# Kernel tuning notes

Measured on AMD Instinct MI355X. Metric: run time of the kernel, lower is better.

Reference implementation:

```python
import jax, jax.numpy as jnp
import numpy as np

NUM_TAGS = 32            # init arg
N = NUM_TAGS + 2         # internal num_tags (start/end appended)
START = N - 2
END = N - 1
B = 1024
T = 1024
NEG = -6969.0            # module's 'minus infinity' constant


def setup_inputs() -> dict:
    key = jax.random.key(0)
    k1, k2 = jax.random.split(key)
    features = jax.random.normal(k1, (B, T, N), dtype=jnp.float32)
    # learned parameter: transition matrix [N, N]
    transitions = jax.random.normal(k2, (N, N), dtype=jnp.float32)
    return {"features": features, "transitions": transitions}


def _viterbi(features, transitions):
    # features: [B, T, N]; transitions: [N, N]
    Bn, Tn, Nn = features.shape
    init = jnp.full((Bn, Nn), NEG, dtype=features.dtype).at[:, START].set(0.0)

    def step(scores, feat):
        # score[b, j, k] = scores[b, k] + feat[b, j] + transitions[j, k]
        sc = scores[:, None, :] + feat[:, :, None] + transitions[None, :, :]
        return jnp.max(sc, axis=-1), jnp.argmax(sc, axis=-1)

    feats_t = jnp.swapaxes(features, 0, 1)            # [T, B, N]
    scores, paths = jax.lax.scan(step, init, feats_t)  # paths: [T, B, N] int

    scores = scores + transitions[END]                # add transition to end tag
    best = jnp.max(scores, axis=-1)                   # [B]
    idx = jnp.argmax(scores, axis=-1)                 # [B]

    # backtrack through backpointers, from t = T-1 down to 0
    def back(i, path):
        ni = jnp.take_along_axis(path, i[:, None], axis=1)[:, 0]
        return ni, ni

    _, tags = jax.lax.scan(back, idx, paths, reverse=True)  # tags: [T, B]
    best_path = jnp.concatenate([tags.T, idx[:, None]], axis=1)  # [B, T+1]
    return best, best_path


def reference(features, transitions):
    return _viterbi(features, transitions)
```

## Files before the change

kernel.cpp:

```cpp
#include <hip/hip_runtime.h>
#include <stdint.h>

#define BB 1024
#define TT 1024
#define NN 34
#define NP 36
#define NB 2
#define TPB (NB * 136)
#define NEGV -6969.0f
#define PADV -1.0e30f

template<int C>
__device__ __forceinline__ int dpp_i(int x) {
    return __builtin_amdgcn_update_dpp(0, x, C, 0xF, 0xF, true);
}
template<int C>
__device__ __forceinline__ float dpp_f(float x) {
    return __int_as_float(dpp_i<C>(__float_as_int(x)));
}

__device__ __forceinline__ void lds_barrier() {
    asm volatile("s_waitcnt lgkmcnt(0)\n\ts_barrier" ::: "memory");
}

__global__ __launch_bounds__(TPB, 3) void viterbi_full(
        const float* __restrict__ feat,
        const float* __restrict__ trans,
        unsigned char* __restrict__ bpg,
        float* __restrict__ out)
{
    __shared__ float sbuf[2][NB][NP];
    __shared__ float fsb[NB][NN];
    __shared__ unsigned char Fm[NB][16][NN];
    __shared__ int Eb[NB][16];
    __shared__ int idxs[NB];

    const int tid = threadIdx.x;
    const int bl  = (tid >= 136) ? 1 : 0;
    const int r   = tid - bl * 136;
    const int j   = r >> 2;
    const int h   = r & 3;
    const int k0  = h * 9;
    const int bg  = blockIdx.x * NB + bl;

    for (int e = tid; e < 2 * NB * NP; e += TPB) {
        int kk = e % NP;
        ((float*)sbuf)[e] = (kk >= NN) ? PADV : ((kk == 32) ? 0.0f : NEGV);
    }

    float tr[9];
    int   kreg[9];
#pragma unroll
    for (int i = 0; i < 9; ++i) {
        int k = k0 + i;
        tr[i]   = (k < NN) ? trans[j * NN + k] : 0.0f;
        kreg[i] = k;
    }
    const float trE = (r < NN) ? trans[33 * NN + r] : 0.0f;

    const float* fp = feat + (size_t)bg * TT * NN + j;
    unsigned char* bpt = bpg + (size_t)bg * TT * NN + j;

    float fr0 = fp[0 * NN], fr1 = fp[1 * NN], fr2 = fp[2 * NN], fr3 = fp[3 * NN];

    float* const s0 = &sbuf[0][bl][0];
    float* const s1 = &sbuf[1][bl][0];

    __syncthreads();

    auto vstep = [&](const float* __restrict__ srd, float* __restrict__ swr,
                     float fv, unsigned char* bpw) {
        float vv[9];
#pragma unroll
        for (int i = 0; i < 9; ++i) vv[i] = (srd[k0 + i] + fv) + tr[i];
        float m = fmaxf(fmaxf(fmaxf(vv[0], vv[1]), fmaxf(vv[2], vv[3])),
                        fmaxf(fmaxf(vv[4], vv[5]), fmaxf(vv[6], vv[7])));
        m = fmaxf(m, vv[8]);
        m = fmaxf(m, dpp_f<0xB1>(m));
        m = fmaxf(m, dpp_f<0x4E>(m));
        int am = 127;
#pragma unroll
        for (int i = 8; i >= 0; --i) am = (vv[i] == m) ? kreg[i] : am;
        int ao = dpp_i<0xB1>(am); am = (ao < am) ? ao : am;
        ao = dpp_i<0x4E>(am);     am = (ao < am) ? ao : am;
        if (h == 0) { swr[j] = m; *bpw = (unsigned char)am; }
        lds_barrier();
    };

    for (int n = 0; n < 255; ++n) {
        { float f = fr0; fr0 = fp[4 * NN]; vstep(s0, s1, f, bpt + 0 * NN); }
        { float f = fr1; fr1 = fp[5 * NN]; vstep(s1, s0, f, bpt + 1 * NN); }
        { float f = fr2; fr2 = fp[6 * NN]; vstep(s0, s1, f, bpt + 2 * NN); }
        { float f = fr3; fr3 = fp[7 * NN]; vstep(s1, s0, f, bpt + 3 * NN); }
        fp += 4 * NN; bpt += 4 * NN;
    }
    vstep(s0, s1, fr0, bpt + 0 * NN);
    vstep(s1, s0, fr1, bpt + 1 * NN);
    vstep(s0, s1, fr2, bpt + 2 * NN);
    vstep(s1, s0, fr3, bpt + 3 * NN);

    if (r < NN) fsb[bl][r] = s0[r] + trE;
    __syncthreads();
    if (r == 0) {
        float bm = fsb[bl][0]; int bi = 0;
        for (int k = 1; k < NN; ++k) {
            float v = fsb[bl][k];
            if (v > bm) { bm = v; bi = k; }
        }
        out[bg] = bm; idxs[bl] = bi;
    }
    __syncthreads();

    const unsigned char* __restrict__ bb = bpg + (size_t)bg * TT * NN;

    {
        int g = (r >= 102) ? 3 : ((r >= 68) ? 2 : ((r >= 34) ? 1 : 0));
        int x = r - 34 * g;
        int c0 = g, c1 = g + 4, c2 = g + 8, c3 = g + 12;
        int m0 = x, m1 = x, m2 = x, m3 = x;
        for (int i = 63; i >= 0; --i) {
            m0 = bb[(size_t)((c0 * 64 + i) * NN) + m0];
            m1 = bb[(size_t)((c1 * 64 + i) * NN) + m1];
            m2 = bb[(size_t)((c2 * 64 + i) * NN) + m2];
            m3 = bb[(size_t)((c3 * 64 + i) * NN) + m3];
        }
        Fm[bl][c0][x] = m0; Fm[bl][c1][x] = m1;
        Fm[bl][c2][x] = m2; Fm[bl][c3][x] = m3;
    }
    __syncthreads();

    if (r == 0) {
        int e = idxs[bl];
        Eb[bl][15] = e;
        for (int c = 15; c >= 1; --c) { e = Fm[bl][c][e]; Eb[bl][c - 1] = e; }
    }
    __syncthreads();

    float* po = out + BB + (size_t)bg * (TT + 1);
    if (r < 16) {
        int c = r;
        int m = Eb[bl][c];
        for (int i = 63; i >= 0; --i) {
            m = bb[(size_t)((c * 64 + i) * NN) + m];
            po[c * 64 + i] = (float)m;
        }
    }
    if (r == 16) po[TT] = (float)idxs[bl];
}

extern "C" void kernel_launch(void* const* d_in, const int* in_sizes, int n_in,
                              void* d_out, int out_size, void* d_ws, size_t ws_size,
                              hipStream_t stream) {
    const float* feat  = (const float*)d_in[0];
    const float* trans = (const float*)d_in[1];
    float* out = (float*)d_out;
    unsigned char* bp = (unsigned char*)d_ws;

    viterbi_full<<<BB / NB, TPB, 0, stream>>>(feat, trans, bp, out);
}
```

Baseline: 547.3 us.

## Defer argmax off the critical path and vectorize LDS score loads

The per-step backpointer argmax is moved into the next step, where it is computed while that step's score loads from LDS are in flight. Only the max and the score write stay on the serial dependency chain between barriers. Each of the four lanes per tag now reads an overlapping 10-wide window at stride 8, fetched with float4/float2 LDS loads, which replaces the 9 scalar loads per lane. This adds registers for the carried previous values, plus a flush after the loop, in exchange for a shorter latency chain per timestep.

```diff
diff --git a/kernel.cpp b/kernel.cpp
--- a/kernel.cpp
+++ b/kernel.cpp
@@ -23,13 +23,15 @@
     asm volatile("s_waitcnt lgkmcnt(0)\n\ts_barrier" ::: "memory");
 }
 
+__device__ __forceinline__ int imin2(int a, int b) { return a < b ? a : b; }
+
 __global__ __launch_bounds__(TPB, 3) void viterbi_full(
         const float* __restrict__ feat,
         const float* __restrict__ trans,
         unsigned char* __restrict__ bpg,
         float* __restrict__ out)
 {
-    __shared__ float sbuf[2][NB][NP];
+    __shared__ __align__(16) float sbuf[2][NB][NP];
     __shared__ float fsb[NB][NN];
     __shared__ unsigned char Fm[NB][16][NN];
     __shared__ int Eb[NB][16];
@@ -40,7 +42,7 @@
     const int r   = tid - bl * 136;
     const int j   = r >> 2;
     const int h   = r & 3;
-    const int k0  = h * 9;
+    const int kw  = h << 3;
     const int bg  = blockIdx.x * NB + bl;
 
     for (int e = tid; e < 2 * NB * NP; e += TPB) {
@@ -48,14 +50,9 @@
         ((float*)sbuf)[e] = (kk >= NN) ? PADV : ((kk == 32) ? 0.0f : NEGV);
     }
 
-    float tr[9];
-    int   kreg[9];
+    float tr[10];
 #pragma unroll
-    for (int i = 0; i < 9; ++i) {
-        int k = k0 + i;
-        tr[i]   = (k < NN) ? trans[j * NN + k] : 0.0f;
-        kreg[i] = k;
-    }
+    for (int i = 0; i < 10; ++i) tr[i] = trans[j * NN + kw + i];
     const float trE = (r < NN) ? trans[33 * NN + r] : 0.0f;
 
     const float* fp = feat + (size_t)bg * TT * NN + j;
@@ -66,24 +63,51 @@
     float* const s0 = &sbuf[0][bl][0];
     float* const s1 = &sbuf[1][bl][0];
 
+    float pvv[10];
+#pragma unroll
+    for (int i = 0; i < 10; ++i) pvv[i] = 0.0f;
+    float pm = -1.0e30f;
+    unsigned char* pbp = bpt;
+
     __syncthreads();
+
+    auto amax_flush = [&]() {
+        int e[10];
+#pragma unroll
+        for (int i = 0; i < 10; ++i) e[i] = (pvv[i] == pm) ? (kw + i) : 127;
+        int a0 = imin2(e[0], e[1]), a1 = imin2(e[2], e[3]);
+        int a2 = imin2(e[4], e[5]), a3 = imin2(e[6], e[7]);
+        int a4 = imin2(e[8], e[9]);
+        int am = imin2(imin2(imin2(a0, a1), imin2(a2, a3)), a4);
+        int ao = dpp_i<0xB1>(am); am = imin2(ao, am);
+        ao = dpp_i<0x4E>(am);     am = imin2(ao, am);
+        if (h == 0) *pbp = (unsigned char)am;
+    };
 
     auto vstep = [&](const float* __restrict__ srd, float* __restrict__ swr,
                      float fv, unsigned char* bpw) {
-        float vv[9];
+        const float4 va = *reinterpret_cast<const float4*>(srd + kw);
+        const float4 vb = *reinterpret_cast<const float4*>(srd + kw + 4);
+        const float2 vc = *reinterpret_cast<const float2*>(srd + kw + 8);
+        amax_flush();
+        float sv[10];
+        sv[0] = va.x; sv[1] = va.y; sv[2] = va.z; sv[3] = va.w;
+        sv[4] = vb.x; sv[5] = vb.y; sv[6] = vb.z; sv[7] = vb.w;
+        sv[8] = vc.x; sv[9] = vc.y;
+        float vv[10];
 #pragma unroll
-        for (int i = 0; i < 9; ++i) vv[i] = (srd[k0 + i] + fv) + tr[i];
-        float m = fmaxf(fmaxf(fmaxf(vv[0], vv[1]), fmaxf(vv[2], vv[3])),
-                        fmaxf(fmaxf(vv[4], vv[5]), fmaxf(vv[6], vv[7])));
-        m = fmaxf(m, vv[8]);
+        for (int i = 0; i < 10; ++i) vv[i] = (sv[i] + fv) + tr[i];
+        float t0 = fmaxf(vv[0], vv[1]), t1 = fmaxf(vv[2], vv[3]);
+        float t2 = fmaxf(vv[4], vv[5]), t3 = fmaxf(vv[6], vv[7]);
+        float t4 = fmaxf(vv[8], vv[9]);
+        float m = fmaxf(fmaxf(fmaxf(t0, t1), fmaxf(t2, t3)), t4);
         m = fmaxf(m, dpp_f<0xB1>(m));
         m = fmaxf(m, dpp_f<0x4E>(m));
-        int am = 127;
+        if (h == 0) swr[j] = m;
 #pragma unroll
-        for (int i = 8; i >= 0; --i) am = (vv[i] == m) ? kreg[i] : am;
-        int ao = dpp_i<0xB1>(am); am = (ao < am) ? ao : am;
-        ao = dpp_i<0x4E>(am);     am = (ao < am) ? ao : am;
-        if (h == 0) { swr[j] = m; *bpw = (unsigned char)am; }
+        for (int i = 0; i < 10; ++i) pvv[i] = vv[i];
+        pm = m;
+        pbp = bpw;
         lds_barrier();
     };
 
@@ -98,6 +122,7 @@
     vstep(s1, s0, fr1, bpt + 1 * NN);
     vstep(s0, s1, fr2, bpt + 2 * NN);
     vstep(s1, s0, fr3, bpt + 3 * NN);
+    amax_flush();
 
     if (r < NN) fsb[bl][r] = s0[r] + trE;
     __syncthreads();
```

After: 561.5 us. +2.6%, slower.

## Map each batch element to one wavefront and drop block barriers from Viterbi scan

Applied to the files above, without the earlier changes.

Restructures the forward Viterbi recursion so a single 64-lane wavefront handles one sequence, with each lane owning one target tag and reducing over all 34 source tags in registers. The old scheme split each tag's reduction across 4 lanes with DPP shuffles and a block-wide barrier per time step. The new scheme exchanges scores through per-wave LDS with no s_barrier, relying on wave-synchronous execution. It also widens the backtrack-composition phase so each lane tracks 9 start tags. This trades roughly four times more ALU work per lane, and idle lanes 34-63, for removing the per-step barrier and cross-lane reductions.

```diff
diff --git a/kernel.cpp b/kernel.cpp
--- a/kernel.cpp
+++ b/kernel.cpp
@@ -4,148 +4,176 @@
 #define BB 1024
 #define TT 1024
 #define NN 34
-#define NP 36
-#define NB 2
-#define TPB (NB * 136)
 #define NEGV -6969.0f
-#define PADV -1.0e30f
 
-template<int C>
-__device__ __forceinline__ int dpp_i(int x) {
-    return __builtin_amdgcn_update_dpp(0, x, C, 0xF, 0xF, true);
-}
-template<int C>
-__device__ __forceinline__ float dpp_f(float x) {
-    return __int_as_float(dpp_i<C>(__float_as_int(x)));
+typedef float v2f __attribute__((ext_vector_type(2)));
+typedef float v4f __attribute__((ext_vector_type(4)));
+
+__device__ __forceinline__ float fmax3(float a, float b, float c) {
+    return fmaxf(fmaxf(a, b), c);
 }
 
-__device__ __forceinline__ void lds_barrier() {
-    asm volatile("s_waitcnt lgkmcnt(0)\n\ts_barrier" ::: "memory");
-}
-
-__global__ __launch_bounds__(TPB, 3) void viterbi_full(
+__global__ __launch_bounds__(256, 1) void viterbi_wave(
         const float* __restrict__ feat,
         const float* __restrict__ trans,
         unsigned char* __restrict__ bpg,
         float* __restrict__ out)
 {
-    __shared__ float sbuf[2][NB][NP];
-    __shared__ float fsb[NB][NN];
-    __shared__ unsigned char Fm[NB][16][NN];
-    __shared__ int Eb[NB][16];
-    __shared__ int idxs[NB];
+    __shared__ __align__(16) float sc[4][64];
+    __shared__ unsigned char Fm[4][16][NN];
+    __shared__ int Eb[4][16];
 
-    const int tid = threadIdx.x;
-    const int bl  = (tid >= 136) ? 1 : 0;
-    const int r   = tid - bl * 136;
-    const int j   = r >> 2;
-    const int h   = r & 3;
-    const int k0  = h * 9;
-    const int bg  = blockIdx.x * NB + bl;
+    const int wid  = threadIdx.x >> 6;
+    const int lane = threadIdx.x & 63;
+    const int j    = lane;
+    const int jm   = (j < NN) ? j : (NN - 1);
+    const bool act = (j < NN);
+    const int bg   = blockIdx.x * 4 + wid;
 
-    for (int e = tid; e < 2 * NB * NP; e += TPB) {
-        int kk = e % NP;
-        ((float*)sbuf)[e] = (kk >= NN) ? PADV : ((kk == 32) ? 0.0f : NEGV);
+    v4f t4[8]; v2f t2;
+    {
+        const float* trow = trans + jm * NN;
+#pragma unroll
+        for (int i = 0; i < 8; ++i)
+            t4[i] = (v4f){trow[4*i], trow[4*i+1], trow[4*i+2], trow[4*i+3]};
+        t2 = (v2f){trow[32], trow[33]};
+    }
+    v4f e4[8]; v2f e2;
+    {
+        const float* erow = trans + (NN - 1) * NN;
+#pragma unroll
+        for (int i = 0; i < 8; ++i)
+            e4[i] = (v4f){erow[4*i], erow[4*i+1], erow[4*i+2], erow[4*i+3]};
+        e2 = (v2f){erow[32], erow[33]};
     }
 
-    float tr[9];
-    int   kreg[9];
-#pragma unroll
-    for (int i = 0; i < 9; ++i) {
-        int k = k0 + i;
-        tr[i]   = (k < NN) ? trans[j * NN + k] : 0.0f;
-        kreg[i] = k;
-    }
-    const float trE = (r < NN) ? trans[33 * NN + r] : 0.0f;
-
-    const float* fp = feat + (size_t)bg * TT * NN + j;
+    const float* fp = feat + (size_t)bg * TT * NN + jm;
     unsigned char* bpt = bpg + (size_t)bg * TT * NN + j;
 
-    float fr0 = fp[0 * NN], fr1 = fp[1 * NN], fr2 = fp[2 * NN], fr3 = fp[3 * NN];
+    float* const scW = &sc[wid][0];
+    const v4f* const S4 = (const v4f*)scW;
+    const v2f* const S2 = (const v2f*)scW;
 
-    float* const s0 = &sbuf[0][bl][0];
-    float* const s1 = &sbuf[1][bl][0];
+    scW[lane] = (lane == 32) ? 0.0f : NEGV;
 
-    __syncthreads();
+    v4f q[8]; v2f q8;
+#pragma unroll
+    for (int i = 0; i < 8; ++i) q[i] = S4[i];
+    q8 = S2[16];
 
-    auto vstep = [&](const float* __restrict__ srd, float* __restrict__ swr,
-                     float fv, unsigned char* bpw) {
-        float vv[9];
+    float fr0 = fp[0*NN], fr1 = fp[1*NN], fr2 = fp[2*NN], fr3 = fp[3*NN];
+
+    auto vstep = [&](float fv, unsigned char* bpw) {
+        const v4f f4 = (v4f){fv, fv, fv, fv};
+        const v2f f2 = (v2f){fv, fv};
+        v4f w[8]; v2f w8;
 #pragma unroll
-        for (int i = 0; i < 9; ++i) vv[i] = (srd[k0 + i] + fv) + tr[i];
-        float m = fmaxf(fmaxf(fmaxf(vv[0], vv[1]), fmaxf(vv[2], vv[3])),
-                        fmaxf(fmaxf(vv[4], vv[5]), fmaxf(vv[6], vv[7])));
-        m = fmaxf(m, vv[8]);
-        m = fmaxf(m, dpp_f<0xB1>(m));
-        m = fmaxf(m, dpp_f<0x4E>(m));
+        for (int i = 0; i < 8; ++i) w[i] = (q[i] + f4) + t4[i];
+        w8 = (q8 + f2) + t2;
+        float wv[NN];
+#pragma unroll
+        for (int i = 0; i < 8; ++i) {
+            wv[4*i+0] = w[i].x; wv[4*i+1] = w[i].y;
+            wv[4*i+2] = w[i].z; wv[4*i+3] = w[i].w;
+        }
+        wv[32] = w8.x; wv[33] = w8.y;
+        float a[12];
+#pragma unroll
+        for (int i = 0; i < 11; ++i) a[i] = fmax3(wv[3*i], wv[3*i+1], wv[3*i+2]);
+        a[11] = wv[33];
+        float b0 = fmax3(a[0], a[1], a[2]), b1 = fmax3(a[3], a[4], a[5]);
+        float b2 = fmax3(a[6], a[7], a[8]), b3 = fmax3(a[9], a[10], a[11]);
+        float m = fmaxf(fmaxf(b0, b1), fmaxf(b2, b3));
+        scW[lane] = m;
+#pragma unroll
+        for (int i = 0; i < 8; ++i) q[i] = S4[i];
+        q8 = S2[16];
         int am = 127;
 #pragma unroll
-        for (int i = 8; i >= 0; --i) am = (vv[i] == m) ? kreg[i] : am;
-        int ao = dpp_i<0xB1>(am); am = (ao < am) ? ao : am;
-        ao = dpp_i<0x4E>(am);     am = (ao < am) ? ao : am;
-        if (h == 0) { swr[j] = m; *bpw = (unsigned char)am; }
-        lds_barrier();
+        for (int k = NN - 1; k >= 0; --k) am = (wv[k] == m) ? k : am;
+        if (act) *bpw = (unsigned char)am;
     };
 
     for (int n = 0; n < 255; ++n) {
-        { float f = fr0; fr0 = fp[4 * NN]; vstep(s0, s1, f, bpt + 0 * NN); }
-        { float f = fr1; fr1 = fp[5 * NN]; vstep(s1, s0, f, bpt + 1 * NN); }
-        { float f = fr2; fr2 = fp[6 * NN]; vstep(s0, s1, f, bpt + 2 * NN); }
-        { float f = fr3; fr3 = fp[7 * NN]; vstep(s1, s0, f, bpt + 3 * NN); }
-        fp += 4 * NN; bpt += 4 * NN;
+        { float f = fr0; fr0 = fp[4*NN]; vstep(f, bpt + 0*NN); }
+        { float f = fr1; fr1 = fp[5*NN]; vstep(f, bpt + 1*NN); }
+        { float f = fr2; fr2 = fp[6*NN]; vstep(f, bpt + 2*NN); }
+        { float f = fr3; fr3 = fp[7*NN]; vstep(f, bpt + 3*NN); }
+        fp += 4*NN; bpt += 4*NN;
     }
-    vstep(s0, s1, fr0, bpt + 0 * NN);
-    vstep(s1, s0, fr1, bpt + 1 * NN);
-    vstep(s0, s1, fr2, bpt + 2 * NN);
-    vstep(s1, s0, fr3, bpt + 3 * NN);
+    vstep(fr0, bpt + 0*NN);
+    vstep(fr1, bpt + 1*NN);
+    vstep(fr2, bpt + 2*NN);
+    vstep(fr3, bpt + 3*NN);
 
-    if (r < NN) fsb[bl][r] = s0[r] + trE;
-    __syncthreads();
-    if (r == 0) {
-        float bm = fsb[bl][0]; int bi = 0;
-        for (int k = 1; k < NN; ++k) {
-            float v = fsb[bl][k];
-            if (v > bm) { bm = v; bi = k; }
+    int bi;
+    float bm;
+    {
+        v4f w[8]; v2f w8;
+#pragma unroll
+        for (int i = 0; i < 8; ++i) w[i] = q[i] + e4[i];
+        w8 = q8 + e2;
+        float wv[NN];
+#pragma unroll
+        for (int i = 0; i < 8; ++i) {
+            wv[4*i+0] = w[i].x; wv[4*i+1] = w[i].y;
+            wv[4*i+2] = w[i].z; wv[4*i+3] = w[i].w;
         }
-        out[bg] = bm; idxs[bl] = bi;
+        wv[32] = w8.x; wv[33] = w8.y;
+        float a[12];
+#pragma unroll
+        for (int i = 0; i < 11; ++i) a[i] = fmax3(wv[3*i], wv[3*i+1], wv[3*i+2]);
+        a[11] = wv[33];
+        float b0 = fmax3(a[0], a[1], a[2]), b1 = fmax3(a[3], a[4], a[5]);
+        float b2 = fmax3(a[6], a[7], a[8]), b3 = fmax3(a[9], a[10], a[11]);
+        bm = fmaxf(fmaxf(b0, b1), fmaxf(b2, b3));
+        bi = 127;
+#pragma unroll
+        for (int k = NN - 1; k >= 0; --k) bi = (wv[k] == bm) ? k : bi;
     }
-    __syncthreads();
+    if (lane == 0) out[bg] = bm;
 
+    asm volatile("s_waitcnt vmcnt(0)" ::: "memory");
     const unsigned char* __restrict__ bb = bpg + (size_t)bg * TT * NN;
 
     {
-        int g = (r >= 102) ? 3 : ((r >= 68) ? 2 : ((r >= 34) ? 1 : 0));
-        int x = r - 34 * g;
-        int c0 = g, c1 = g + 4, c2 = g + 8, c3 = g + 12;
-        int m0 = x, m1 = x, m2 = x, m3 = x;
+        const int c = lane >> 2;
+        const int sub = lane & 3;
+        int mv[9];
+#pragma unroll
+        for (int qi = 0; qi < 9; ++qi) {
+            int x = sub + 4 * qi;
+            mv[qi] = (x < NN) ? x : (NN - 1);
+        }
+        const unsigned char* cb = bb + (size_t)c * 64 * NN;
         for (int i = 63; i >= 0; --i) {
-            m0 = bb[(size_t)((c0 * 64 + i) * NN) + m0];
-            m1 = bb[(size_t)((c1 * 64 + i) * NN) + m1];
-            m2 = bb[(size_t)((c2 * 64 + i) * NN) + m2];
-            m3 = bb[(size_t)((c3 * 64 + i) * NN) + m3];
+            const unsigned char* rb = cb + (size_t)i * NN;
+#pragma unroll
+            for (int qi = 0; qi < 9; ++qi) mv[qi] = rb[mv[qi]];
         }
-        Fm[bl][c0][x] = m0; Fm[bl][c1][x] = m1;
-        Fm[bl][c2][x] = m2; Fm[bl][c3][x] = m3;
+#pragma unroll
+        for (int qi = 0; qi < 9; ++qi) {
+            int x = sub + 4 * qi;
+            if (x < NN) Fm[wid][c][x] = (unsigned char)mv[qi];
+        }
     }
-    __syncthreads();
 
-    if (r == 0) {
-        int e = idxs[bl];
-        Eb[bl][15] = e;
-        for (int c = 15; c >= 1; --c) { e = Fm[bl][c][e]; Eb[bl][c - 1] = e; }
+    if (lane == 0) {
+        int e = bi;
+        Eb[wid][15] = e;
+        for (int c = 15; c >= 1; --c) { e = Fm[wid][c][e]; Eb[wid][c - 1] = e; }
     }
-    __syncthreads();
 
     float* po = out + BB + (size_t)bg * (TT + 1);
-    if (r < 16) {
-        int c = r;
-        int m = Eb[bl][c];
+    if (lane < 16) {
+        int c = lane;
+        int m = Eb[wid][c];
         for (int i = 63; i >= 0; --i) {
             m = bb[(size_t)((c * 64 + i) * NN) + m];
             po[c * 64 + i] = (float)m;
         }
     }
-    if (r == 16) po[TT] = (float)idxs[bl];
+    if (lane == 16) po[TT] = (float)bi;
 }
 
 extern "C" void kernel_launch(void* const* d_in, const int* in_sizes, int n_in,
@@ -156,5 +184,5 @@
     float* out = (float*)d_out;
     unsigned char* bp = (unsigned char*)d_ws;
 
-    viterbi_full<<<BB / NB, TPB, 0, stream>>>(feat, trans, bp, out);
+    viterbi_wave<<<BB / 4, 256, 0, stream>>>(feat, trans, bp, out);
 }
```

After: 626.8 us. 1.15x slower.

## Process two batch rows per thread instead of per thread group

Applied to the files above, without the earlier changes.

Before, each block ran 272 threads, one 136-thread group per batch row. Now each block has 136 threads and every thread handles both rows, interleaving their independent max/argmax chains inside each step. This is meant to halve the threads per batch and give each thread two independent dependency chains to hide LDS and DPP latency. The cost is roughly double the register use per thread (launch bounds lowered from 3 to 2) and longer per-step work on the serial critical path.

```diff
diff --git a/kernel.cpp b/kernel.cpp
--- a/kernel.cpp
+++ b/kernel.cpp
@@ -6,7 +6,7 @@
 #define NN 34
 #define NP 36
 #define NB 2
-#define TPB (NB * 136)
+#define TPB 136
 #define NEGV -6969.0f
 #define PADV -1.0e30f
 
@@ -23,7 +23,7 @@
     asm volatile("s_waitcnt lgkmcnt(0)\n\ts_barrier" ::: "memory");
 }
 
-__global__ __launch_bounds__(TPB, 3) void viterbi_full(
+__global__ __launch_bounds__(TPB, 2) void viterbi_full(
         const float* __restrict__ feat,
         const float* __restrict__ trans,
         unsigned char* __restrict__ bpg,
@@ -35,15 +35,13 @@
     __shared__ int Eb[NB][16];
     __shared__ int idxs[NB];
 
-    const int tid = threadIdx.x;
-    const int bl  = (tid >= 136) ? 1 : 0;
-    const int r   = tid - bl * 136;
+    const int r   = threadIdx.x;
     const int j   = r >> 2;
     const int h   = r & 3;
     const int k0  = h * 9;
-    const int bg  = blockIdx.x * NB + bl;
+    const int bg0 = blockIdx.x * NB;
 
-    for (int e = tid; e < 2 * NB * NP; e += TPB) {
+    for (int e = r; e < 2 * NB * NP; e += TPB) {
         int kk = e % NP;
         ((float*)sbuf)[e] = (kk >= NN) ? PADV : ((kk == 32) ? 0.0f : NEGV);
     }
@@ -58,94 +56,131 @@
     }
     const float trE = (r < NN) ? trans[33 * NN + r] : 0.0f;
 
-    const float* fp = feat + (size_t)bg * TT * NN + j;
-    unsigned char* bpt = bpg + (size_t)bg * TT * NN + j;
+    const float* fpb[NB];
+    unsigned char* bptb[NB];
+#pragma unroll
+    for (int b = 0; b < NB; ++b) {
+        fpb[b]  = feat + (size_t)(bg0 + b) * TT * NN + j;
+        bptb[b] = bpg  + (size_t)(bg0 + b) * TT * NN + j;
+    }
 
-    float fr0 = fp[0 * NN], fr1 = fp[1 * NN], fr2 = fp[2 * NN], fr3 = fp[3 * NN];
-
-    float* const s0 = &sbuf[0][bl][0];
-    float* const s1 = &sbuf[1][bl][0];
+    float fr0[NB], fr1[NB], fr2[NB], fr3[NB];
+#pragma unroll
+    for (int b = 0; b < NB; ++b) {
+        fr0[b] = fpb[b][0 * NN]; fr1[b] = fpb[b][1 * NN];
+        fr2[b] = fpb[b][2 * NN]; fr3[b] = fpb[b][3 * NN];
+    }
 
     __syncthreads();
 
-    auto vstep = [&](const float* __restrict__ srd, float* __restrict__ swr,
-                     float fv, unsigned char* bpw) {
-        float vv[9];
-#pragma unroll
-        for (int i = 0; i < 9; ++i) vv[i] = (srd[k0 + i] + fv) + tr[i];
-        float m = fmaxf(fmaxf(fmaxf(vv[0], vv[1]), fmaxf(vv[2], vv[3])),
-                        fmaxf(fmaxf(vv[4], vv[5]), fmaxf(vv[6], vv[7])));
-        m = fmaxf(m, vv[8]);
-        m = fmaxf(m, dpp_f<0xB1>(m));
-        m = fmaxf(m, dpp_f<0x4E>(m));
-        int am = 127;
-#pragma unroll
-        for (int i = 8; i >= 0; --i) am = (vv[i] == m) ? kreg[i] : am;
-        int ao = dpp_i<0xB1>(am); am = (ao < am) ? ao : am;
-        ao = dpp_i<0x4E>(am);     am = (ao < am) ? ao : am;
-        if (h == 0) { swr[j] = m; *bpw = (unsigned char)am; }
-        lds_barrier();
-    };
+#define VSTEP(SRD, SWR, FRQ, QOFF, PF)                                        \
+    {                                                                         \
+        float fv_[NB];                                                        \
+        _Pragma("unroll") for (int b = 0; b < NB; ++b) {                      \
+            fv_[b] = FRQ[b];                                                  \
+            if (PF) FRQ[b] = fpb[b][(4 + QOFF) * NN];                         \
+        }                                                                     \
+        float vv_[NB][9];                                                     \
+        _Pragma("unroll") for (int b = 0; b < NB; ++b) {                      \
+            const float* srd_ = &sbuf[SRD][b][0];                            \
+            _Pragma("unroll") for (int i = 0; i < 9; ++i)                     \
+                vv_[b][i] = (srd_[k0 + i] + fv_[b]) + tr[i];                  \
+        }                                                                     \
+        _Pragma("unroll") for (int b = 0; b < NB; ++b) {                      \
+            float m_ = fmaxf(fmaxf(fmaxf(vv_[b][0], vv_[b][1]),               \
+                                   fmaxf(vv_[b][2], vv_[b][3])),              \
+                             fmaxf(fmaxf(vv_[b][4], vv_[b][5]),               \
+                                   fmaxf(vv_[b][6], vv_[b][7])));             \
+            m_ = fmaxf(m_, vv_[b][8]);                                        \
+            m_ = fmaxf(m_, dpp_f<0xB1>(m_));                  \
+            m_ = fmaxf(m_, dpp_f<0x4E>(m_));                  \
+            int am_ = 127;                                                    \
+            _Pragma("unroll") for (int i = 8; i >= 0; --i)                    \
+                am_ = (vv_[b][i] == m_) ? kreg[i] : am_;                      \
+            int ao_ = dpp_i<0xB1>(am_); am_ = (ao_ < am_) ? ao_ : am_;        \
+            ao_ = dpp_i<0x4E>(am_);     am_ = (ao_ < am_) ? ao_ : am_;        \
+            if (h == 0) { sbuf[SWR][b][j] = m_;                               \
+                          bptb[b][QOFF * NN] = (unsigned char)am_; }          \
+        }                                                                     \
+        lds_barrier();                                                        \
+    }
 
     for (int n = 0; n < 255; ++n) {
-        { float f = fr0; fr0 = fp[4 * NN]; vstep(s0, s1, f, bpt + 0 * NN); }
-        { float f = fr1; fr1 = fp[5 * NN]; vstep(s1, s0, f, bpt + 1 * NN); }
-        { float f = fr2; fr2 = fp[6 * NN]; vstep(s0, s1, f, bpt + 2 * NN); }
-        { float f = fr3; fr3 = fp[7 * NN]; vstep(s1, s0, f, bpt + 3 * NN); }
-        fp += 4 * NN; bpt += 4 * NN;
+        VSTEP(0, 1, fr0, 0, true)
+        VSTEP(1, 0, fr1, 1, true)
+        VSTEP(0, 1, fr2, 2, true)
+        VSTEP(1, 0, fr3, 3, true)
+#pragma unroll
+        for (int b = 0; b < NB; ++b) { fpb[b] += 4 * NN; bptb[b] += 4 * NN; }
     }
-    vstep(s0, s1, fr0, bpt + 0 * NN);
-    vstep(s1, s0, fr1, bpt + 1 * NN);
-    vstep(s0, s1, fr2, bpt + 2 * NN);
-    vstep(s1, s0, fr3, bpt + 3 * NN);
+    VSTEP(0, 1, fr0, 0, false)
+    VSTEP(1, 0, fr1, 1, false)
+    VSTEP(0, 1, fr2, 2, false)
+    VSTEP(1, 0, fr3, 3, false)
 
-    if (r < NN) fsb[bl][r] = s0[r] + trE;
+#pragma unroll
+    for (int b = 0; b < NB; ++b)
+        if (r < NN) fsb[b][r] = sbuf[0][b][r] + trE;
     __syncthreads();
-    if (r == 0) {
-        float bm = fsb[bl][0]; int bi = 0;
+    if (r < NB) {
+        const int b = r;
+        float bm = fsb[b][0]; int bi = 0;
         for (int k = 1; k < NN; ++k) {
-            float v = fsb[bl][k];
+            float v = fsb[b][k];
             if (v > bm) { bm = v; bi = k; }
         }
-        out[bg] = bm; idxs[bl] = bi;
+        out[bg0 + b] = bm; idxs[b] = bi;
     }
     __syncthreads();
-
-    const unsigned char* __restrict__ bb = bpg + (size_t)bg * TT * NN;
 
     {
         int g = (r >= 102) ? 3 : ((r >= 68) ? 2 : ((r >= 34) ? 1 : 0));
         int x = r - 34 * g;
-        int c0 = g, c1 = g + 4, c2 = g + 8, c3 = g + 12;
-        int m0 = x, m1 = x, m2 = x, m3 = x;
+        int mv[NB][4];
+#pragma unroll
+        for (int b = 0; b < NB; ++b)
+#pragma unroll
+            for (int cc = 0; cc < 4; ++cc) mv[b][cc] = x;
         for (int i = 63; i >= 0; --i) {
-            m0 = bb[(size_t)((c0 * 64 + i) * NN) + m0];
-            m1 = bb[(size_t)((c1 * 64 + i) * NN) + m1];
-            m2 = bb[(size_t)((c2 * 64 + i) * NN) + m2];
-            m3 = bb[(size_t)((c3 * 64 + i) * NN) + m3];
+#pragma unroll
+            for (int b = 0; b < NB; ++b) {
+                const unsigned char* bbb = bpg + (size_t)(bg0 + b) * TT * NN;
+#pragma unroll
+                for (int cc = 0; cc < 4; ++cc) {
+                    int c = g + 4 * cc;
+                    mv[b][cc] = bbb[(size_t)((c * 64 + i) * NN) + mv[b][cc]];
+                }
+            }
         }
-        Fm[bl][c0][x] = m0; Fm[bl][c1][x] = m1;
-        Fm[bl][c2][x] = m2; Fm[bl][c3][x] = m3;
+#pragma unroll
+        for (int b = 0; b < NB; ++b)
+#pragma unroll
+            for (int cc = 0; cc < 4; ++cc) Fm[b][g + 4 * cc][x] = mv[b][cc];
     }
     __syncthreads();
 
-    if (r == 0) {
-        int e = idxs[bl];
-        Eb[bl][15] = e;
-        for (int c = 15; c >= 1; --c) { e = Fm[bl][c][e]; Eb[bl][c - 1] = e; }
+    if (r < NB) {
+        const int b = r;
+        int e = idxs[b];
+        Eb[b][15] = e;
+        for (int c = 15; c >= 1; --c) { e = Fm[b][c][e]; Eb[b][c - 1] = e; }
     }
     __syncthreads();
 
-    float* po = out + BB + (size_t)bg * (TT + 1);
-    if (r < 16) {
-        int c = r;
-        int m = Eb[bl][c];
+    if (r < 16 * NB) {
+        const int b = r >> 4, c = r & 15;
+        const unsigned char* bbb = bpg + (size_t)(bg0 + b) * TT * NN;
+        float* po = out + BB + (size_t)(bg0 + b) * (TT + 1);
+        int m = Eb[b][c];
         for (int i = 63; i >= 0; --i) {
-            m = bb[(size_t)((c * 64 + i) * NN) + m];
+            m = bbb[(size_t)((c * 64 + i) * NN) + m];
             po[c * 64 + i] = (float)m;
         }
     }
-    if (r == 16) po[TT] = (float)idxs[bl];
+    if (r >= 16 * NB && r < 16 * NB + NB) {
+        const int b = r - 16 * NB;
+        (out + BB + (size_t)(bg0 + b) * (TT + 1))[TT] = (float)idxs[b];
+    }
 }
 
 extern "C" void kernel_launch(void* const* d_in, const int* in_sizes, int n_in,
```

Result: slower. 752.5 us (+37.5%).
